# Performance work log

Measured on AMD Instinct MI355X. Metric: run time of the kernel, lower is better.

## Reference

```python
import jax, jax.numpy as jnp
import numpy as np

C_CURV = 1.0
SQRT_C = C_CURV ** 0.5
MAX_NORM = 1.0 / SQRT_C - 1e-5  # project eps == dist clamp eps == 1e-5
EPS = 1e-15


def setup_inputs() -> dict:
    key = jax.random.key(0)
    k1, k2 = jax.random.split(key)
    B, C, D = 4096, 8192, 256
    # points well inside the unit ball: ||x|| ~ 0.05*sqrt(D) ~ 0.8
    x = jax.random.normal(k1, (B, D), dtype=jnp.float32) * 0.05
    # matches nn.Parameter(torch.randn(C, D) * 0.01)
    proto_tangent = jax.random.normal(k2, (C, D), dtype=jnp.float32) * 0.01
    log_scale = jnp.zeros((C,), dtype=jnp.float32)
    return {"x": x, "proto_tangent": proto_tangent, "log_scale": log_scale}


def _expmap0_project(v):
    # exp_0(v) = tanh(sqrt(c)||v||) v / (sqrt(c)||v||), then project onto ball
    vn = jnp.maximum(jnp.linalg.norm(v, axis=-1, keepdims=True), EPS)
    p = jnp.tanh(SQRT_C * vn) * v / (SQRT_C * vn)
    pn = jnp.linalg.norm(p, axis=-1, keepdims=True)
    return jnp.where(pn > MAX_NORM, p / pn * MAX_NORM, p)


def reference(x, proto_tangent, log_scale):
    protos = _expmap0_project(proto_tangent)          # [C, D]
    c = C_CURV
    # mobius_add(-x, y) broadcast over [B, C]; we only need its norm, so use
    # ||a*(-x) + b*y||^2 = a^2||x||^2 - 2ab<x,y> + b^2||y||^2 (same math,
    # avoids materializing the [B, C, D] intermediate the torch code builds).
    x2 = jnp.sum(x * x, axis=-1)[:, None]             # [B, 1]
    y2 = jnp.sum(protos * protos, axis=-1)[None, :]   # [1, C]
    xy = x @ protos.T                                  # [B, C]  <x, y>
    nxy = -xy                                          # <-x, y>
    a = 1.0 + 2.0 * c * nxy + c * y2                   # coeff of (-x)
    b = 1.0 - c * x2                                   # coeff of y
    denom = jnp.maximum(1.0 + 2.0 * c * nxy + (c * c) * x2 * y2, EPS)
    num_sq = a * a * x2 + 2.0 * a * b * nxy + b * b * y2
    norm = jnp.sqrt(jnp.maximum(num_sq, 0.0)) / denom  # ||mobius_add(-x,y)||
    # project clamp (eps=1e-5) and dist clamp (1/sqrt(c)-1e-5) coincide
    norm = jnp.minimum(norm, MAX_NORM)
    dists = (2.0 / SQRT_C) * jnp.arctanh(SQRT_C * norm)  # [B, C]
    return -dists * jnp.exp(log_scale)[None, :]
```

## Files before the change

kernel.cpp:

```cpp
#include <hip/hip_runtime.h>
#include <hip/hip_bf16.h>
#include <cstdint>

#define MAX_NORM (1.0f - 1e-5f)
#define LN2 0.69314718056f
#define WMAX ((1.0f + MAX_NORM) / (1.0f - MAX_NORM))

typedef __attribute__((ext_vector_type(8))) short bf16x8;
typedef __attribute__((ext_vector_type(4))) float f32x4;

__device__ __forceinline__ unsigned short f2bf(float f) {
  union { float f; unsigned int u; } c; c.f = f;
  unsigned int r = c.u + 0x7fffu + ((c.u >> 16) & 1u);
  return (unsigned short)(r >> 16);
}

__device__ __forceinline__ void gld16(const unsigned short* g, unsigned short* l) {
  __builtin_amdgcn_global_load_lds(
      (const __attribute__((address_space(1))) unsigned int*)g,
      (__attribute__((address_space(3))) unsigned int*)l, 16, 0, 0);
}

__global__ void prep_all(const float* __restrict__ x, const float* __restrict__ pt,
                         const float* __restrict__ ls,
                         unsigned short* __restrict__ xbf, unsigned short* __restrict__ pbf,
                         float* __restrict__ x2, float* __restrict__ fx,
                         float* __restrict__ gy, float* __restrict__ hy,
                         float* __restrict__ es2, int M, int N, int D) {
  int row = blockIdx.x * (blockDim.x >> 6) + (threadIdx.x >> 6);
  int lane = threadIdx.x & 63;
  if (row >= M + N) return;
  const bool isX = row < M;
  const int r = isX ? row : row - M;
  const float* src = (isX ? x : pt) + (size_t)r * D;
  f32x4 v = ((const f32x4*)src)[lane];
  float ss = v[0]*v[0] + v[1]*v[1] + v[2]*v[2] + v[3]*v[3];
  #pragma unroll
  for (int off = 32; off >= 1; off >>= 1) ss += __shfl_xor(ss, off);
  float scale = 1.0f;
  float outsq = ss;
  if (!isX) {
    float vn  = sqrtf(ss);
    float vnc = fmaxf(vn, 1e-15f);
    float th  = tanhf(vnc);
    scale = th / vnc;
    float pn = scale * vn;
    if (pn > MAX_NORM) { float pr = MAX_NORM / pn; scale *= pr; pn = MAX_NORM; }
    outsq = pn * pn;
  }
  unsigned short* dst = (isX ? xbf : pbf) + (size_t)r * D + lane * 4;
  unsigned long long pk =
        (unsigned long long)f2bf(v[0]*scale)
      | ((unsigned long long)f2bf(v[1]*scale) << 16)
      | ((unsigned long long)f2bf(v[2]*scale) << 32)
      | ((unsigned long long)f2bf(v[3]*scale) << 48);
  *(unsigned long long*)dst = pk;
  if (lane == 0) {
    if (isX) {
      x2[r] = outsq;
      fx[r] = 2.0f / (1.0f - outsq);
    } else {
      float g = 1.0f / (1.0f - outsq);
      gy[r]  = g;
      hy[r]  = g * outsq;
      es2[r] = -__expf(ls[r]) * LN2;
    }
  }
}

__global__ __launch_bounds__(256, 2)
void hyp_gemm(const unsigned short* __restrict__ xbf,
              const unsigned short* __restrict__ pbf,
              const float* __restrict__ x2, const float* __restrict__ fx,
              const float* __restrict__ gy, const float* __restrict__ hy,
              const float* __restrict__ es2, float* __restrict__ out,
              int M, int N, int K) {
  __shared__ __align__(16) unsigned short As[2][2][128 * 32];
  __shared__ __align__(16) unsigned short Bs[2][2][128 * 32];
  const int t    = threadIdx.x;
  const int wv   = t >> 6;
  const int lane = t & 63;
  const int wr   = wv >> 1, wc = wv & 1;
  const int frow = lane & 15, kgrp = lane >> 4;
  const int nTM  = M >> 7;
  const int tileM  = blockIdx.x % nTM;
  const int tileN0 = (blockIdx.x / nTM) * 4;
  const int gr0 = tileM * 128 + wr * 64;

  f32x4 accA[4][4], accB[4][4];

  const int srow  = wv * 16 + (lane >> 2);
  const int skoff = (lane & 3) * 8;
  const unsigned short* gA  = xbf + (size_t)(tileM * 128 + srow) * K + skoff;
  const unsigned short* gB0 = pbf + (size_t)(tileN0 * 128 + srow) * K + skoff;
  const size_t rskip = (size_t)64 * K;
  const size_t nskip = (size_t)128 * K;

  float x2s[4], fxs[4];
  #pragma unroll
  for (int m = 0; m < 4; ++m) {
    x2s[m] = x2[gr0 + m * 16 + frow];
    fxs[m] = fx[gr0 + m * 16 + frow];
  }

#define STAGE(b, kt, GBP)                                                      \
  {                                                                            \
    _Pragma("unroll")                                                          \
    for (int p = 0; p < 2; ++p) {                                              \
      _Pragma("unroll")                                                        \
      for (int j = 0; j < 2; ++j) {                                            \
        gld16(gA + (size_t)j * rskip + (kt) * 64 + p * 32,                     \
              &As[b][p][(j * 64 + wv * 16) * 32]);                             \
        gld16((GBP) + (size_t)j * rskip + (kt) * 64 + p * 32,                  \
              &Bs[b][p][(j * 64 + wv * 16) * 32]);                             \
      }                                                                        \
    }                                                                          \
  }

#define COMPUTE(b, ACC)                                                        \
  {                                                                            \
    __builtin_amdgcn_s_setprio(1);                                             \
    _Pragma("unroll")                                                          \
    for (int p = 0; p < 2; ++p) {                                              \
      bf16x8 af[4], bg[4];                                                     \
      _Pragma("unroll")                                                        \
      for (int m = 0; m < 4; ++m)                                              \
        af[m] = *(const bf16x8*)&As[b][p][(wr * 64 + m * 16 + frow) * 32 + kgrp * 8]; \
      _Pragma("unroll")                                                        \
      for (int n = 0; n < 4; ++n)                                              \
        bg[n] = *(const bf16x8*)&Bs[b][p][(wc * 64 + n * 16 + frow) * 32 + kgrp * 8]; \
      _Pragma("unroll")                                                        \
      for (int m = 0; m < 4; ++m)                                              \
        _Pragma("unroll")                                                      \
        for (int n = 0; n < 4; ++n)                                            \
          ACC[m][n] = __builtin_amdgcn_mfma_f32_16x16x32_bf16(bg[n], af[m], ACC[m][n], 0, 0, 0); \
    }                                                                          \
    __builtin_amdgcn_s_setprio(0);                                             \
  }

#define EPI_SLICE(ACC, TNP, NN)                                                \
  {                                                                            \
    const int c0 = (tileN0 + (TNP)) * 128 + wc * 64 + (NN) * 16 + kgrp * 4;    \
    f32x4 gv = *(const f32x4*)(gy  + c0);                                      \
    f32x4 hv = *(const f32x4*)(hy  + c0);                                      \
    f32x4 ev = *(const f32x4*)(es2 + c0);                                      \
    _Pragma("unroll")                                                          \
    for (int m = 0; m < 4; ++m) {                                              \
      f32x4 a4 = ACC[m][(NN)];                                                 \
      f32x4 o;                                                                 \
      _Pragma("unroll")                                                        \
      for (int r = 0; r < 4; ++r) {                                            \
        float xy = a4[r];                                                      \
        float u  = fmaf(fxs[m], fmaf(gv[r], fmaf(-2.0f, xy, x2s[m]), hv[r]), 1.0f); \
        float t2 = fmaxf(fmaf(u, u, -1.0f), 0.0f);                             \
        float w  = fminf(u + __builtin_amdgcn_sqrtf(t2), WMAX);                \
        o[r] = ev[r] * __log2f(w);                                             \
      }                                                                        \
      *(f32x4*)&out[(size_t)(gr0 + m * 16 + frow) * N + c0] = o;               \
    }                                                                          \
  }

#define TILE(TN, ACCC, ACCP)                                                   \
  {                                                                            \
    _Pragma("unroll")                                                          \
    for (int m = 0; m < 4; ++m)                                                \
      _Pragma("unroll")                                                        \
      for (int n = 0; n < 4; ++n) ACCC[m][n] = (f32x4){0.f, 0.f, 0.f, 0.f};    \
    __syncthreads();                                                           \
    _Pragma("unroll")                                                          \
    for (int kt = 0; kt < 4; ++kt) {                                           \
      if (kt < 3)          STAGE(cur ^ 1, kt + 1, gB0 + (TN) * nskip)          \
      else if ((TN) < 3)   STAGE(cur ^ 1, 0, gB0 + ((TN) + 1) * nskip)         \
      if ((TN) > 0)        EPI_SLICE(ACCP, (TN) - 1, kt)                       \
      COMPUTE(cur, ACCC)                                                       \
      __syncthreads();                                                         \
      cur ^= 1;                                                                \
    }                                                                          \
  }

  STAGE(0, 0, gB0)
  int cur = 0;
  TILE(0, accA, accB)
  TILE(1, accB, accA)
  TILE(2, accA, accB)
  TILE(3, accB, accA)
  #pragma unroll
  for (int n = 0; n < 4; ++n) EPI_SLICE(accB, 3, n)

#undef TILE
#undef EPI_SLICE
#undef COMPUTE
#undef STAGE
}

extern "C" void kernel_launch(void* const* d_in, const int* in_sizes, int n_in,
                              void* d_out, int out_size, void* d_ws, size_t ws_size,
                              hipStream_t stream) {
  const float* x  = (const float*)d_in[0];
  const float* pt = (const float*)d_in[1];
  const float* ls = (const float*)d_in[2];
  const int Csz = in_sizes[2];
  const int D   = in_sizes[1] / Csz;
  const int Bsz = in_sizes[0] / D;
  const int M = Bsz, N = Csz, K = D;
  float* outp = (float*)d_out;

  char* ws = (char*)d_ws;
  unsigned short* xbf = (unsigned short*)ws; ws += (size_t)M * K * 2;
  unsigned short* pbf = (unsigned short*)ws; ws += (size_t)N * K * 2;
  float* x2  = (float*)ws; ws += (size_t)M * 4;
  float* fx  = (float*)ws; ws += (size_t)M * 4;
  float* gy  = (float*)ws; ws += (size_t)N * 4;
  float* hy  = (float*)ws; ws += (size_t)N * 4;
  float* es2 = (float*)ws; ws += (size_t)N * 4;

  hipLaunchKernelGGL(prep_all, dim3((M + N + 3) / 4), dim3(256), 0, stream,
                     x, pt, ls, xbf, pbf, x2, fx, gy, hy, es2, M, N, K);
  hipLaunchKernelGGL(hyp_gemm, dim3((M / 128) * (N / 512)), dim3(256), 0, stream,
                     xbf, pbf, x2, fx, gy, hy, es2, outp, M, N, K);
}
```

Before: 52.96 us.

## Reorder pipeline: issue stage loads after compute, prefetch epilogue params, use explicit vmcnt waits

Restructures the per-k-step loop so the next global->LDS stage is issued after the MFMA compute. The epilogue's gy/hy/es2 vectors are prefetched one step ahead into registers and the split epilogue consumes them. The full __syncthreads is replaced by a partial s_waitcnt vmcnt(3) plus s_barrier, so the prefetched epilogue loads can stay in flight across the barrier. This relies on the exact count of outstanding vector memory ops being correct. A miscount could race on the LDS buffers or read epilogue values before they arrive.

```diff
diff --git a/kernel.cpp b/kernel.cpp
--- a/kernel.cpp
+++ b/kernel.cpp
@@ -20,6 +20,9 @@
       (const __attribute__((address_space(1))) unsigned int*)g,
       (__attribute__((address_space(3))) unsigned int*)l, 16, 0, 0);
 }
+
+#define WVM0 asm volatile("s_waitcnt vmcnt(0)" ::: "memory")
+#define WVM3 asm volatile("s_waitcnt vmcnt(3)" ::: "memory")
 
 __global__ void prep_all(const float* __restrict__ x, const float* __restrict__ pt,
                          const float* __restrict__ ls,
@@ -88,6 +91,7 @@
   const int gr0 = tileM * 128 + wr * 64;
 
   f32x4 accA[4][4], accB[4][4];
+  f32x4 e_gv, e_hv, e_ev;
 
   const int srow  = wv * 16 + (lane >> 2);
   const int skoff = (lane & 3) * 8;
@@ -138,23 +142,27 @@
     __builtin_amdgcn_s_setprio(0);                                             \
   }
 
-#define EPI_SLICE(ACC, TNP, NN)                                                \
+#define EPI_LOAD(TNP, NN)                                                      \
   {                                                                            \
     const int c0 = (tileN0 + (TNP)) * 128 + wc * 64 + (NN) * 16 + kgrp * 4;    \
-    f32x4 gv = *(const f32x4*)(gy  + c0);                                      \
-    f32x4 hv = *(const f32x4*)(hy  + c0);                                      \
-    f32x4 ev = *(const f32x4*)(es2 + c0);                                      \
+    e_gv = *(const f32x4*)(gy  + c0);                                          \
+    e_hv = *(const f32x4*)(hy  + c0);                                          \
+    e_ev = *(const f32x4*)(es2 + c0);                                          \
+  }
+
+#define EPI_STORE(ACC, TNP, NN)                                                \
+  {                                                                            \
+    const int c0 = (tileN0 + (TNP)) * 128 + wc * 64 + (NN) * 16 + kgrp * 4;    \
     _Pragma("unroll")                                                          \
     for (int m = 0; m < 4; ++m) {                                              \
       f32x4 a4 = ACC[m][(NN)];                                                 \
       f32x4 o;                                                                 \
       _Pragma("unroll")                                                        \
       for (int r = 0; r < 4; ++r) {                                            \
-        float xy = a4[r];                                                      \
-        float u  = fmaf(fxs[m], fmaf(gv[r], fmaf(-2.0f, xy, x2s[m]), hv[r]), 1.0f); \
+        float u  = fmaf(fxs[m], fmaf(e_gv[r], fmaf(-2.0f, a4[r], x2s[m]), e_hv[r]), 1.0f); \
         float t2 = fmaxf(fmaf(u, u, -1.0f), 0.0f);                             \
         float w  = fminf(u + __builtin_amdgcn_sqrtf(t2), WMAX);                \
-        o[r] = ev[r] * __log2f(w);                                             \
+        o[r] = e_ev[r] * __log2f(w);                                           \
       }                                                                        \
       *(f32x4*)&out[(size_t)(gr0 + m * 16 + frow) * N + c0] = o;               \
     }                                                                          \
@@ -166,14 +174,16 @@
     for (int m = 0; m < 4; ++m)                                                \
       _Pragma("unroll")                                                        \
       for (int n = 0; n < 4; ++n) ACCC[m][n] = (f32x4){0.f, 0.f, 0.f, 0.f};    \
-    __syncthreads();                                                           \
     _Pragma("unroll")                                                          \
     for (int kt = 0; kt < 4; ++kt) {                                           \
-      if (kt < 3)          STAGE(cur ^ 1, kt + 1, gB0 + (TN) * nskip)          \
-      else if ((TN) < 3)   STAGE(cur ^ 1, 0, gB0 + ((TN) + 1) * nskip)         \
-      if ((TN) > 0)        EPI_SLICE(ACCP, (TN) - 1, kt)                       \
+      if ((TN) > 0) { WVM3; } else { WVM0; }                                   \
+      __builtin_amdgcn_s_barrier();                                            \
+      if ((TN) > 0) EPI_STORE(ACCP, (TN) - 1, kt)                              \
       COMPUTE(cur, ACCC)                                                       \
-      __syncthreads();                                                         \
+      if (kt < 3)        STAGE(cur ^ 1, kt + 1, gB0 + (TN) * nskip)            \
+      else if ((TN) < 3) STAGE(cur ^ 1, 0, gB0 + ((TN) + 1) * nskip)           \
+      if (kt < 3) { if ((TN) > 0) EPI_LOAD((TN) - 1, kt + 1) }                 \
+      else          EPI_LOAD((TN), 0)                                          \
       cur ^= 1;                                                                \
     }                                                                          \
   }
@@ -184,11 +194,14 @@
   TILE(1, accB, accA)
   TILE(2, accA, accB)
   TILE(3, accB, accA)
-  #pragma unroll
-  for (int n = 0; n < 4; ++n) EPI_SLICE(accB, 3, n)
+  EPI_STORE(accB, 3, 0) EPI_LOAD(3, 1)
+  EPI_STORE(accB, 3, 1) EPI_LOAD(3, 2)
+  EPI_STORE(accB, 3, 2) EPI_LOAD(3, 3)
+  EPI_STORE(accB, 3, 3)
 
 #undef TILE
-#undef EPI_SLICE
+#undef EPI_LOAD
+#undef EPI_STORE
 #undef COMPUTE
 #undef STAGE
 }
```

Result: faster. 51.77 us (-2.2%).
